# Kernel optimization log

Measured on AMD Instinct MI355X. Metric: run time of the kernel, lower is better.

Reference implementation:

```python
import jax, jax.numpy as jnp
import numpy as np

HIDDEN = 256


def setup_inputs() -> dict:
    key = jax.random.key(0)
    ks = jax.random.split(key, 7)
    B, T, H = 16384, 1024, HIDDEN
    s_ih = 1.0 / np.sqrt(H)
    x = jax.random.normal(ks[0], (B, T), dtype=jnp.float32)
    # GRU cell params (PyTorch GRUCell layout: gates ordered r, z, n)
    w_ih = jax.random.uniform(ks[1], (3 * H, 1), jnp.float32, -s_ih, s_ih)
    w_hh = jax.random.uniform(ks[2], (3 * H, H), jnp.float32, -s_ih, s_ih)
    b_ih = jax.random.uniform(ks[3], (3 * H,), jnp.float32, -s_ih, s_ih)
    b_hh = jax.random.uniform(ks[4], (3 * H,), jnp.float32, -s_ih, s_ih)
    # output head Linear(H, 1)
    w_out = jax.random.uniform(ks[5], (1, H), jnp.float32, -s_ih, s_ih)
    b_out = jax.random.uniform(ks[6], (1,), jnp.float32, -s_ih, s_ih)
    return {"x": x, "w_ih": w_ih, "w_hh": w_hh, "b_ih": b_ih,
            "b_hh": b_hh, "w_out": w_out, "b_out": b_out}


def reference(x, w_ih, w_hh, b_ih, b_hh, w_out, b_out):
    B, T = x.shape
    H = w_hh.shape[1]
    h0 = jnp.zeros((B, H), dtype=x.dtype)
    wi = w_ih[:, 0]  # [3H], input dim is 1

    def step(h, x_t):
        # x_t: [B]; gi: [B, 3H]; gh: [B, 3H]
        gi = x_t[:, None] * wi[None, :] + b_ih
        gh = h @ w_hh.T + b_hh
        gi_r, gi_z, gi_n = jnp.split(gi, 3, axis=1)
        gh_r, gh_z, gh_n = jnp.split(gh, 3, axis=1)
        r = jax.nn.sigmoid(gi_r + gh_r)
        z = jax.nn.sigmoid(gi_z + gh_z)
        n = jnp.tanh(gi_n + r * gh_n)
        h_new = (1.0 - z) * n + z * h
        out_t = jax.nn.relu(h_new) @ w_out.T + b_out  # [B, 1]
        return h_new, out_t[:, 0]

    _, outs = jax.lax.scan(step, h0, x.T)  # outs: [T, B]
    return outs.T  # [B, T]
```

## Files before the change

kernel.cpp:

```cpp
#include <hip/hip_runtime.h>


#define B_TOTAL 16384
#define T_LEN   1024
#define GRPROWS 16
#define M_ROWS  32
#define NBLOCKS (B_TOTAL / M_ROWS)
#define NTHREADS 512
#define LDSW    264

typedef short short8 __attribute__((ext_vector_type(8)));
typedef float f32x4  __attribute__((ext_vector_type(4)));

__device__ unsigned short g_wsw[196608];

__device__ __forceinline__ unsigned short f2b(float f) {
  unsigned u = __builtin_bit_cast(unsigned, f);
  u += 0x7fffu + ((u >> 16) & 1u);
  return (unsigned short)(u >> 16);
}
__device__ __forceinline__ unsigned cvt_pk_bf16(float lo, float hi) {
  unsigned r;
  asm("v_cvt_pk_bf16_f32 %0, %1, %2" : "=v"(r) : "v"(lo), "v"(hi));
  return r;
}
__device__ __forceinline__ float dpp_red16(float v) {
  int x = __builtin_bit_cast(int, v);
  v += __builtin_bit_cast(float, __builtin_amdgcn_update_dpp(0, x, 0x118, 0xF, 0xF, true));
  x = __builtin_bit_cast(int, v);
  v += __builtin_bit_cast(float, __builtin_amdgcn_update_dpp(0, x, 0x114, 0xF, 0xF, true));
  x = __builtin_bit_cast(int, v);
  v += __builtin_bit_cast(float, __builtin_amdgcn_update_dpp(0, x, 0x112, 0xF, 0xF, true));
  x = __builtin_bit_cast(int, v);
  v += __builtin_bit_cast(float, __builtin_amdgcn_update_dpp(0, x, 0x111, 0xF, 0xF, true));
  return v;
}
__device__ __forceinline__ void barrier_lgkm() {
  asm volatile("s_waitcnt lgkmcnt(0)\n\ts_barrier" ::: "memory");
}

__global__ void prep_w(const float* __restrict__ w_hh) {
  int tid  = blockIdx.x * 256 + threadIdx.x;
  int e    = tid & 7;
  int lane = (tid >> 3) & 63;
  int ks   = (tid >> 9) & 7;
  int nt   = tid >> 12;
  int row  = nt * 16 + (lane & 15);
  int col  = ks * 32 + (lane >> 4) * 8 + e;
  float s  = (row < 512) ? -1.44269504f : 2.88539008f;
  g_wsw[tid] = f2b(w_hh[row * 256 + col] * s);
}

#define MF(A, B, C) __builtin_amdgcn_mfma_f32_16x16x32_bf16((A), (B), (C), 0, 0, 0)

#define KSTEP(P, AR, KS, EXTRA)  {                                             \
    short8 a_  = *(const short8*)((AR) + (KS)*32);                             \
    short8 z1_ = *(const short8*)&w_lds[wz1b + (KS)*512];                      \
    short8 n1_ = *(const short8*)&w_lds[wn1b + (KS)*512];                      \
    P##00 = MF(a_, wrr0[KS], P##00);                                           \
    P##01 = MF(a_, wrr1[KS], P##01);                                           \
    P##10 = MF(a_, wrz0[KS], P##10);                                           \
    P##11 = MF(a_, z1_,      P##11);                                           \
    P##20 = MF(a_, wrn0[KS], P##20);                                           \
    P##21 = MF(a_, n1_,      P##21);                                           \
    EXTRA                                                                      \
  }

#define GEL(AC, HR, XV, VO, J, I) {                                            \
    float t_r = __builtin_fmaf(XV[I], swr[J], AC##0##J[I]);                    \
    float rg_ = __builtin_amdgcn_rcpf(1.0f + __builtin_amdgcn_exp2f(t_r));     \
    float t_z = __builtin_fmaf(XV[I], swz[J], AC##1##J[I]);                    \
    float zg_ = __builtin_amdgcn_rcpf(1.0f + __builtin_amdgcn_exp2f(t_z));     \
    float t_n = __builtin_fmaf(XV[I], swn[J], sbni[J]);                        \
    float yn_ = __builtin_fmaf(rg_, AC##2##J[I], t_n);                         \
    float rn_ = __builtin_amdgcn_rcpf(1.0f + __builtin_amdgcn_exp2f(yn_));     \
    float ng_ = __builtin_fmaf(-2.0f, rn_, 1.0f);                              \
    float hn_ = __builtin_fmaf(zg_, HR[J][I] - ng_, ng_);                      \
    HR[J][I] = hn_;                                                            \
    VO[I] += fmaxf(hn_, 0.0f)*wo[J];                                           \
  }

#define PUBP(HR, HG, J, I0) {                                                  \
    unsigned pk_ = cvt_pk_bf16(HR[J][I0], HR[J][(I0)+1]);                      \
    h_lds[HG][hwb[J] + (I0)*LDSW]     = (unsigned short)pk_;                   \
    h_lds[HG][hwb[J] + ((I0)+1)*LDSW] = (unsigned short)(pk_ >> 16);           \
  }

#define VORED(VO, G, S) {                                                      \
    _Pragma("unroll") for (int i_ = 0; i_ < 4; ++i_) VO[i_] = dpp_red16(VO[i_]); \
    if (r16 == 15) {                                                           \
      _Pragma("unroll") for (int i_ = 0; i_ < 4; ++i_)                         \
        op[G][(S)&1][w][q*4 + i_] = VO[i_];                                    \
    } }

#define FIN(G, S, TLO)                                                         \
  if (tid >= (TLO) && tid < (TLO) + 16) {                                      \
    float o_ = bo;                                                             \
    _Pragma("unroll") for (int ww_ = 0; ww_ < 8; ++ww_)                        \
      o_ += op[G][(S)&1][ww_][tid - (TLO)];                                    \
    out[(base + (G)*GRPROWS + (tid - (TLO)))*T_LEN + (S)] = o_;                \
  }

#define ACCB(P) {                                                              \
    P##00 = (f32x4){sbr[0],sbr[0],sbr[0],sbr[0]};                              \
    P##01 = (f32x4){sbr[1],sbr[1],sbr[1],sbr[1]};                              \
    P##10 = (f32x4){sbz[0],sbz[0],sbz[0],sbz[0]};                              \
    P##11 = (f32x4){sbz[1],sbz[1],sbz[1],sbz[1]};                              \
    P##20 = (f32x4){sbnh[0],sbnh[0],sbnh[0],sbnh[0]};                          \
    P##21 = (f32x4){sbnh[1],sbnh[1],sbnh[1],sbnh[1]};                          \
  }

#define XLOAD(XV, G, S) {                                                      \
    _Pragma("unroll") for (int i_ = 0; i_ < 4; ++i_)                           \
      XV[i_] = x[(base + (G)*GRPROWS + q*4 + i_)*T_LEN + (S)];                 \
  }

__global__ __launch_bounds__(NTHREADS, 2) void gru_kernel(
    const float* __restrict__ x,
    const float* __restrict__ w_ih,
    const float* __restrict__ b_ih,
    const float* __restrict__ b_hh,
    const float* __restrict__ w_out,
    const float* __restrict__ b_out,
    float* __restrict__ out)
{
  __shared__ unsigned short h_lds[2][GRPROWS * LDSW];
  __shared__ unsigned short w_lds[16 * 8 * 512];
  __shared__ float op[2][2][8][GRPROWS];

  const int tid  = threadIdx.x;
  const int w    = tid >> 6;
  const int lane = tid & 63;
  const int r16  = lane & 15;
  const int q    = lane >> 4;
  const long base = (long)blockIdx.x * M_ROWS;

  for (int i = tid; i < 2 * GRPROWS * LDSW; i += NTHREADS) h_lds[0][i] = 0;

  const int wz1b = ((w*2 + 0)*8)*512 + lane*8;
  const int wn1b = ((w*2 + 1)*8)*512 + lane*8;
#pragma unroll
  for (int gsel = 0; gsel < 2; ++gsel)
#pragma unroll
    for (int ks = 0; ks < 8; ++ks)
      *(short8*)&w_lds[((w*2 + gsel)*8 + ks)*512 + lane*8] =
        *(const short8*)&g_wsw[((((gsel + 1)*16 + w*2 + 1)*8 + ks)*64 + lane)*8];

  short8 wrr0[8], wrr1[8], wrz0[8], wrn0[8];
#pragma unroll
  for (int ks = 0; ks < 8; ++ks) {
    wrr0[ks] = *(const short8*)&g_wsw[(((0*16 + w*2 + 0)*8 + ks)*64 + lane)*8];
    wrr1[ks] = *(const short8*)&g_wsw[(((0*16 + w*2 + 1)*8 + ks)*64 + lane)*8];
    wrz0[ks] = *(const short8*)&g_wsw[(((1*16 + w*2 + 0)*8 + ks)*64 + lane)*8];
    wrn0[ks] = *(const short8*)&g_wsw[(((2*16 + w*2 + 0)*8 + ks)*64 + lane)*8];
  }

  const float C1 = 1.44269504f;
  float swr[2], swz[2], swn[2], sbr[2], sbz[2], sbni[2], sbnh[2], wo[2];
  int cc[2], hwb[2];
#pragma unroll
  for (int j = 0; j < 2; ++j) {
    int c = w*32 + j*16 + r16;
    cc[j]    = c;
    hwb[j]   = (q*4)*LDSW + c;
    swr[j]   = -C1 * w_ih[c];
    swz[j]   = -C1 * w_ih[256 + c];
    swn[j]   = 2.0f * C1 * w_ih[512 + c];
    sbr[j]   = -C1 * (b_ih[c]       + b_hh[c]);
    sbz[j]   = -C1 * (b_ih[256 + c] + b_hh[256 + c]);
    sbni[j]  = 2.0f * C1 * b_ih[512 + c];
    sbnh[j]  = 2.0f * C1 * b_hh[512 + c];
    wo[j]    = w_out[c];
  }
  const float bo = b_out[0];
  const f32x4 zero4 = {0.f, 0.f, 0.f, 0.f};

  float hP[2][4], hQ[2][4];
#pragma unroll
  for (int j = 0; j < 2; ++j)
#pragma unroll
    for (int i = 0; i < 4; ++i) { hP[j][i] = 0.0f; hQ[j][i] = 0.0f; }

  const unsigned short* arP = &h_lds[0][r16*LDSW + q*8];
  const unsigned short* arQ = &h_lds[1][r16*LDSW + q*8];

  f32x4 aP00, aP01, aP10, aP11, aP20, aP21;
  f32x4 aQ00, aQ01, aQ10, aQ11, aQ20, aQ21;

  barrier_lgkm();

  {
    ACCB(aP)
    KSTEP(aP, arP, 0, ) KSTEP(aP, arP, 1, ) KSTEP(aP, arP, 2, ) KSTEP(aP, arP, 3, )
    KSTEP(aP, arP, 4, ) KSTEP(aP, arP, 5, ) KSTEP(aP, arP, 6, ) KSTEP(aP, arP, 7, )
    barrier_lgkm();
  }

#pragma unroll 1
  for (int s = 0; s < T_LEN - 1; ++s) {
    {
      f32x4 xvP; XLOAD(xvP, 0, s);
      if (s > 0) { FIN(0, s-1, 0) }
      ACCB(aQ)
      f32x4 voP = zero4;
      KSTEP(aQ, arQ, 0, GEL(aP, hP, xvP, voP, 0, 0))
      KSTEP(aQ, arQ, 1, GEL(aP, hP, xvP, voP, 0, 1) PUBP(hP, 0, 0, 0))
      KSTEP(aQ, arQ, 2, GEL(aP, hP, xvP, voP, 0, 2))
      KSTEP(aQ, arQ, 3, GEL(aP, hP, xvP, voP, 0, 3) PUBP(hP, 0, 0, 2))
      KSTEP(aQ, arQ, 4, GEL(aP, hP, xvP, voP, 1, 0))
      KSTEP(aQ, arQ, 5, GEL(aP, hP, xvP, voP, 1, 1) PUBP(hP, 0, 1, 0))
      KSTEP(aQ, arQ, 6, GEL(aP, hP, xvP, voP, 1, 2))
      KSTEP(aQ, arQ, 7, GEL(aP, hP, xvP, voP, 1, 3) PUBP(hP, 0, 1, 2))
      VORED(voP, 0, s)
      barrier_lgkm();
    }
    {
      f32x4 xvQ; XLOAD(xvQ, 1, s);
      if (s > 0) { FIN(1, s-1, 64) }
      ACCB(aP)
      f32x4 voQ = zero4;
      KSTEP(aP, arP, 0, GEL(aQ, hQ, xvQ, voQ, 0, 0))
      KSTEP(aP, arP, 1, GEL(aQ, hQ, xvQ, voQ, 0, 1) PUBP(hQ, 1, 0, 0))
      KSTEP(aP, arP, 2, GEL(aQ, hQ, xvQ, voQ, 0, 2))
      KSTEP(aP, arP, 3, GEL(aQ, hQ, xvQ, voQ, 0, 3) PUBP(hQ, 1, 0, 2))
      KSTEP(aP, arP, 4, GEL(aQ, hQ, xvQ, voQ, 1, 0))
      KSTEP(aP, arP, 5, GEL(aQ, hQ, xvQ, voQ, 1, 1) PUBP(hQ, 1, 1, 0))
      KSTEP(aP, arP, 6, GEL(aQ, hQ, xvQ, voQ, 1, 2))
      KSTEP(aP, arP, 7, GEL(aQ, hQ, xvQ, voQ, 1, 3) PUBP(hQ, 1, 1, 2))
      VORED(voQ, 1, s)
      barrier_lgkm();
    }
  }

  {
    const int s = T_LEN - 1;
    f32x4 xvP; XLOAD(xvP, 0, s);
    FIN(0, s-1, 0)
    ACCB(aQ)
    f32x4 voP = zero4;
    KSTEP(aQ, arQ, 0, GEL(aP, hP, xvP, voP, 0, 0))
    KSTEP(aQ, arQ, 1, GEL(aP, hP, xvP, voP, 0, 1) PUBP(hP, 0, 0, 0))
    KSTEP(aQ, arQ, 2, GEL(aP, hP, xvP, voP, 0, 2))
    KSTEP(aQ, arQ, 3, GEL(aP, hP, xvP, voP, 0, 3) PUBP(hP, 0, 0, 2))
    KSTEP(aQ, arQ, 4, GEL(aP, hP, xvP, voP, 1, 0))
    KSTEP(aQ, arQ, 5, GEL(aP, hP, xvP, voP, 1, 1) PUBP(hP, 0, 1, 0))
    KSTEP(aQ, arQ, 6, GEL(aP, hP, xvP, voP, 1, 2))
    KSTEP(aQ, arQ, 7, GEL(aP, hP, xvP, voP, 1, 3) PUBP(hP, 0, 1, 2))
    VORED(voP, 0, s)
    barrier_lgkm();
  }
  {
    const int s = T_LEN - 1;
    f32x4 xvQ; XLOAD(xvQ, 1, s);
    FIN(1, s-1, 64)
    f32x4 voQ = zero4;
    GEL(aQ, hQ, xvQ, voQ, 0, 0)
    GEL(aQ, hQ, xvQ, voQ, 0, 1)
    GEL(aQ, hQ, xvQ, voQ, 0, 2)
    GEL(aQ, hQ, xvQ, voQ, 0, 3)
    GEL(aQ, hQ, xvQ, voQ, 1, 0)
    GEL(aQ, hQ, xvQ, voQ, 1, 1)
    GEL(aQ, hQ, xvQ, voQ, 1, 2)
    GEL(aQ, hQ, xvQ, voQ, 1, 3)
    VORED(voQ, 1, s)
    barrier_lgkm();
  }
  FIN(0, T_LEN - 1, 0)
  FIN(1, T_LEN - 1, 64)
}

extern "C" void kernel_launch(void* const* d_in, const int* in_sizes, int n_in,
                              void* d_out, int out_size, void* d_ws, size_t ws_size,
                              hipStream_t stream) {
  const float* x     = (const float*)d_in[0];
  const float* w_ih  = (const float*)d_in[1];
  const float* w_hh  = (const float*)d_in[2];
  const float* b_ih  = (const float*)d_in[3];
  const float* b_hh  = (const float*)d_in[4];
  const float* w_out = (const float*)d_in[5];
  const float* b_out = (const float*)d_in[6];
  float* out = (float*)d_out;

  prep_w<<<768, 256, 0, stream>>>(w_hh);
  gru_kernel<<<NBLOCKS, NTHREADS, 0, stream>>>(x, w_ih, b_ih, b_hh, w_out, b_out, out);
}
```

Measured before the change: 7.945 ms.

## Stage input x through double-buffered LDS in 32-timestep chunks

Replaces the per-step strided global loads of x (four scalar loads per lane, each a row apart) with a cooperative chunked load of 32 timesteps per row into a double-buffered LDS tile. The next chunk is prefetched into registers early in a step and written to the alternate buffer before the barrier. The aim is to take uncoalesced, latency-bound global reads off the recurrent critical path. In exchange it adds a small amount of LDS, a few registers and a branch per step.

```diff
diff --git a/kernel.cpp b/kernel.cpp
--- a/kernel.cpp
+++ b/kernel.cpp
@@ -8,6 +8,9 @@
 #define NBLOCKS (B_TOTAL / M_ROWS)
 #define NTHREADS 512
 #define LDSW    264
+#define TCH     32
+#define NCH     (T_LEN / TCH)
+#define XSTR    36
 
 typedef short short8 __attribute__((ext_vector_type(8)));
 typedef float f32x4  __attribute__((ext_vector_type(4)));
@@ -110,10 +113,8 @@
     P##21 = (f32x4){sbnh[1],sbnh[1],sbnh[1],sbnh[1]};                          \
   }
 
-#define XLOAD(XV, G, S) {                                                      \
-    _Pragma("unroll") for (int i_ = 0; i_ < 4; ++i_)                           \
-      XV[i_] = x[(base + (G)*GRPROWS + q*4 + i_)*T_LEN + (S)];                 \
-  }
+#define XREAD(XV, G, XP, TR)                                                   \
+  XV = *(const f32x4*)&x_buf[XP][(TR)*XSTR + (G)*GRPROWS + q*4];
 
 __global__ __launch_bounds__(NTHREADS, 2) void gru_kernel(
     const float* __restrict__ x,
@@ -127,6 +128,7 @@
   __shared__ unsigned short h_lds[2][GRPROWS * LDSW];
   __shared__ unsigned short w_lds[16 * 8 * 512];
   __shared__ float op[2][2][8][GRPROWS];
+  __shared__ float x_buf[2][TCH * XSTR];
 
   const int tid  = threadIdx.x;
   const int w    = tid >> 6;
@@ -157,11 +159,10 @@
 
   const float C1 = 1.44269504f;
   float swr[2], swz[2], swn[2], sbr[2], sbz[2], sbni[2], sbnh[2], wo[2];
-  int cc[2], hwb[2];
+  int hwb[2];
 #pragma unroll
   for (int j = 0; j < 2; ++j) {
     int c = w*32 + j*16 + r16;
-    cc[j]    = c;
     hwb[j]   = (q*4)*LDSW + c;
     swr[j]   = -C1 * w_ih[c];
     swz[j]   = -C1 * w_ih[256 + c];
@@ -184,6 +185,12 @@
   const unsigned short* arP = &h_lds[0][r16*LDSW + q*8];
   const unsigned short* arQ = &h_lds[1][r16*LDSW + q*8];
 
+  const int xrow = tid >> 5;
+  const int xts  = tid & 31;
+
+  x_buf[0][xts*XSTR + xrow]           = x[(base + xrow)*T_LEN + xts];
+  x_buf[0][xts*XSTR + GRPROWS + xrow] = x[(base + GRPROWS + xrow)*T_LEN + xts];
+
   f32x4 aP00, aP01, aP10, aP11, aP20, aP21;
   f32x4 aQ00, aQ01, aQ10, aQ11, aQ20, aQ21;
 
@@ -198,8 +205,19 @@
 
 #pragma unroll 1
   for (int s = 0; s < T_LEN - 1; ++s) {
+    const int tr = s & (TCH - 1);
+    const int tc = s >> 5;
+    const int xp = tc & 1;
+    const int refill = (tr == 1) && (tc + 1 < NCH);
+
     {
-      f32x4 xvP; XLOAD(xvP, 0, s);
+      float xa, xb;
+      if (refill) {
+        const long t2 = (long)(tc + 1)*TCH + xts;
+        xa = x[(base + xrow)*T_LEN + t2];
+        xb = x[(base + GRPROWS + xrow)*T_LEN + t2];
+      }
+      f32x4 xvP; XREAD(xvP, 0, xp, tr)
       if (s > 0) { FIN(0, s-1, 0) }
       ACCB(aQ)
       f32x4 voP = zero4;
@@ -212,10 +230,14 @@
       KSTEP(aQ, arQ, 6, GEL(aP, hP, xvP, voP, 1, 2))
       KSTEP(aQ, arQ, 7, GEL(aP, hP, xvP, voP, 1, 3) PUBP(hP, 0, 1, 2))
       VORED(voP, 0, s)
+      if (refill) {
+        x_buf[xp ^ 1][xts*XSTR + xrow]           = xa;
+        x_buf[xp ^ 1][xts*XSTR + GRPROWS + xrow] = xb;
+      }
       barrier_lgkm();
     }
     {
-      f32x4 xvQ; XLOAD(xvQ, 1, s);
+      f32x4 xvQ; XREAD(xvQ, 1, xp, tr)
       if (s > 0) { FIN(1, s-1, 64) }
       ACCB(aP)
       f32x4 voQ = zero4;
@@ -234,7 +256,7 @@
 
   {
     const int s = T_LEN - 1;
-    f32x4 xvP; XLOAD(xvP, 0, s);
+    f32x4 xvP; XREAD(xvP, 0, 1, TCH - 1)
     FIN(0, s-1, 0)
     ACCB(aQ)
     f32x4 voP = zero4;
@@ -251,7 +273,7 @@
   }
   {
     const int s = T_LEN - 1;
-    f32x4 xvQ; XLOAD(xvQ, 1, s);
+    f32x4 xvQ; XREAD(xvQ, 1, 1, TCH - 1)
     FIN(1, s-1, 64)
     f32x4 voQ = zero4;
     GEL(aQ, hQ, xvQ, voQ, 0, 0)
```

Result: faster. 7.706 ms (-3.0%).
